# Kernel tuning notes

Measured on AMD Instinct MI355X. Metric: run time of the kernel, lower is better.

## Reference

```python
import jax, jax.numpy as jnp
import numpy as np

CODEBOOK_SIZE = 8192
D_LATENT = 512
COMMITMENT_COST = 0.25


def setup_inputs() -> dict:
    key = jax.random.key(0)
    k1, k2 = jax.random.split(key)
    z = jax.random.normal(k1, (4, 2048, D_LATENT), dtype=jnp.float32)
    # embedding initialized uniform(-1/K, 1/K) in the original; scale a normal draw similarly
    W = jax.random.uniform(k2, (CODEBOOK_SIZE, D_LATENT), dtype=jnp.float32,
                           minval=-1.0 / CODEBOOK_SIZE, maxval=1.0 / CODEBOOK_SIZE)
    return {"z": z, "W": W}


def reference(z, W):
    # Eval-mode forward (no EMA buffer mutation): quantize, straight-through, losses.
    B, S, D = z.shape
    K = W.shape[0]
    z_flat = z.reshape(-1, D)  # [N, D]

    # squared-euclidean distances: ||z||^2 - 2 z W^T + ||w||^2  -> [N, K]
    distances = (jnp.sum(z_flat * z_flat, axis=-1, keepdims=True)
                 - 2.0 * (z_flat @ W.T)
                 + jnp.sum(W * W, axis=-1))
    indices = jnp.argmin(distances, axis=-1)  # [N] int
    z_q = W[indices]  # [N, D] gather

    commitment_loss = jnp.mean((z_flat - jax.lax.stop_gradient(z_q)) ** 2)

    # straight-through estimator
    quantized = z_flat + jax.lax.stop_gradient(z_q - z_flat)

    # perplexity over codebook usage
    counts = jnp.zeros((K,), dtype=jnp.float32).at[indices].add(1.0)
    avg_probs = counts / z_flat.shape[0]
    perplexity = jnp.exp(-jnp.sum(avg_probs * jnp.log(avg_probs + 1e-10)))

    quantized = quantized.reshape(B, S, D)
    indices = indices.reshape(B, S)
    return (quantized, indices, COMMITMENT_COST * commitment_loss, perplexity)
```

## Files before the change

### kernel.cpp

```cpp
#include <hip/hip_runtime.h>
#include <math.h>


typedef __attribute__((ext_vector_type(8))) _Float16 f16x8;
typedef __attribute__((ext_vector_type(16))) float f32x16;

constexpr int N_ROWS = 8192;
constexpr int K_CODES = 8192;
constexpr int D_DIM = 512;
constexpr float COMMIT = 0.25f;
constexpr float EPS = 3.0e-4f;

constexpr size_t OFF_LOSS    = 0;
constexpr size_t OFF_COUNTS  = 64;
constexpr size_t OFF_PARTIAL = 8256;
constexpr size_t OFF_ZZ      = 16384;
constexpr size_t OFF_WW      = 24576;
constexpr size_t OFF_BESTD   = 32768;
constexpr size_t OFF_BESTI   = 2129920;
constexpr size_t F16_BASE_BYTES = 16908288;
constexpr size_t SPLIT_ELEMS = (size_t)8192 * 512;
constexpr size_t SPLIT_BYTES = SPLIT_ELEMS * 2;
constexpr size_t WS_NEED = F16_BASE_BYTES + 2 * SPLIT_BYTES;

constexpr int SPLITK = 8;
constexpr int KSPL = K_CODES / SPLITK;

#define MFMA16(a, b, c) __builtin_amdgcn_mfma_f32_32x32x16_f16((a), (b), (c), 0, 0, 0)

__device__ __forceinline__ bool lexless(float da, int ia, float db, int ib) {
  return da < db || (da == db && ia < ib);
}

__global__ __launch_bounds__(256) void prep_kernel(
    const float* __restrict__ z, const float* __restrict__ W,
    unsigned short* __restrict__ zh, unsigned short* __restrict__ wh,
    float* __restrict__ ws_f) {
  const int src = blockIdx.y;
  const int tid = threadIdx.x;
  if (src == 0 && blockIdx.x < 11) {
#pragma unroll
    for (int k = 0; k < 4; k++) {
      const int idx = blockIdx.x * 1024 + k * 256 + tid;
      if (idx < 10304) ws_f[idx] = 0.0f;
    }
  }
  const float* S = src ? W : z;
  unsigned short* H = src ? wh : zh;
  const float scale = src ? 8192.0f : 1.0f;
  float* norm = ws_f + (src ? OFF_WW : OFF_ZZ);

  const int row = blockIdx.x * 64 + (tid >> 2);
  const int q = tid & 3;
  const float* sp = S + (size_t)row * D_DIM + q * 128;
  const size_t tbase = (size_t)(row >> 7) * 16 * 4096 + (size_t)(row & 127) * 8;

  float4 ssv = {0.f, 0.f, 0.f, 0.f};
#pragma unroll
  for (int c = 0; c < 16; c++) {
    const float4 x = *(const float4*)&sp[c * 8];
    const float4 y = *(const float4*)&sp[c * 8 + 4];
    ssv.x += x.x * x.x; ssv.y += x.y * x.y; ssv.z += x.z * x.z; ssv.w += x.w * x.w;
    ssv.x += y.x * y.x; ssv.y += y.y * y.y; ssv.z += y.z * y.z; ssv.w += y.w * y.w;
    f16x8 hv;
    hv[0] = (_Float16)(x.x * scale); hv[1] = (_Float16)(x.y * scale);
    hv[2] = (_Float16)(x.z * scale); hv[3] = (_Float16)(x.w * scale);
    hv[4] = (_Float16)(y.x * scale); hv[5] = (_Float16)(y.y * scale);
    hv[6] = (_Float16)(y.z * scale); hv[7] = (_Float16)(y.w * scale);
    const int d = q * 128 + c * 8;
    const int dt = d >> 5;
    const int chunk = (d >> 3) & 3;
    *(f16x8*)&H[tbase + (size_t)dt * 4096 + (size_t)chunk * 1024] = hv;
  }
  float s = (ssv.x + ssv.y) + (ssv.z + ssv.w);
  s += __shfl_xor(s, 1, 64);
  s += __shfl_xor(s, 2, 64);
  if (q == 0) norm[row] = s;
}

__global__ __launch_bounds__(256, 2) void vq_screen_kernel(
    const unsigned short* __restrict__ zh_s, const unsigned short* __restrict__ wh_s,
    const float* __restrict__ ww,
    float* __restrict__ bestd2, int* __restrict__ besti2) {
  const int tid = threadIdx.x;
  const int bid = blockIdx.x;
  const int xcd = bid & 7;
  const int j = bid >> 3;
  const int stid = xcd * 8 + (j >> 6);
  const int wi = j & 63;
  const int cb = (stid & 7) * 8 + (wi & 7);
  const int rb = (stid >> 3) * 8 + (wi >> 3);

  const int lane = tid & 63, wv = tid >> 6;
  const int wr = wv >> 1, wc = wv & 1;
  const int lrow = lane & 31, lhi = lane >> 5;

  const f16x8* zh8 = (const f16x8*)zh_s;
  const f16x8* wh8 = (const f16x8*)wh_s;
  const int wbase = wr * 64 + lrow;
  const int zbase = wc * 64 + lrow;

  f32x16 acc[2][2];
#pragma unroll
  for (int i = 0; i < 2; i++)
#pragma unroll
    for (int jj = 0; jj < 2; jj++)
#pragma unroll
      for (int e = 0; e < 16; e++) acc[i][jj][e] = 0.0f;

  f16x8 wA[4], zA[4], wB[4], zB[4];

#define LOADB(WX, ZX, dt) { \
    const int wt_ = (cb * 16 + (dt)) * 512; \
    const int zt_ = (rb * 16 + (dt)) * 512; \
    _Pragma("unroll") \
    for (int ks = 0; ks < 2; ks++) { \
      const int ch_ = ks * 2 + lhi; \
      WX[ks*2+0] = wh8[wt_ + ch_*128 + wbase]; \
      WX[ks*2+1] = wh8[wt_ + ch_*128 + wbase + 32]; \
      ZX[ks*2+0] = zh8[zt_ + ch_*128 + zbase]; \
      ZX[ks*2+1] = zh8[zt_ + ch_*128 + zbase + 32]; \
    } }

#define COMPUTEB(WX, ZX) { \
    __builtin_amdgcn_s_setprio(1); \
    _Pragma("unroll") \
    for (int ks = 0; ks < 2; ks++) { \
      acc[0][0] = MFMA16(WX[ks*2+0], ZX[ks*2+0], acc[0][0]); \
      acc[0][1] = MFMA16(WX[ks*2+0], ZX[ks*2+1], acc[0][1]); \
      acc[1][0] = MFMA16(WX[ks*2+1], ZX[ks*2+0], acc[1][0]); \
      acc[1][1] = MFMA16(WX[ks*2+1], ZX[ks*2+1], acc[1][1]); \
    } \
    __builtin_amdgcn_s_setprio(0); }

  LOADB(wA, zA, 0);
#pragma unroll
  for (int dtp = 0; dtp < 8; dtp++) {
    LOADB(wB, zB, dtp * 2 + 1);
    COMPUTEB(wA, zA);
    if (dtp < 7) LOADB(wA, zA, dtp * 2 + 2);
    COMPUTEB(wB, zB);
  }
#undef LOADB
#undef COMPUTEB

#pragma unroll
  for (int cf = 0; cf < 2; cf++) {
    float p1d = 3.4e38f, p2d = 3.4e38f;
    int   p1i = 0x7fffffff, p2i = 0x7fffffff;
#pragma unroll
    for (int rf = 0; rf < 2; rf++) {
      const int cbase = cb * 128 + wr * 64 + rf * 32 + 4 * lhi;
#pragma unroll
      for (int reg = 0; reg < 16; reg++) {
        const int ci = cbase + (reg & 3) + 8 * (reg >> 2);
        const float d = fmaf(acc[rf][cf][reg], -2.44140625e-4f, ww[ci]);
        const bool b1 = d < p1d;
        const bool b2 = d < p2d;
        p2d = b1 ? p1d : (b2 ? d : p2d);
        p2i = b1 ? p1i : (b2 ? ci : p2i);
        p1d = b1 ? d : p1d;
        p1i = b1 ? ci : p1i;
      }
    }
    const float q1d = __shfl_xor(p1d, 32, 64); const int q1i = __shfl_xor(p1i, 32, 64);
    const float q2d = __shfl_xor(p2d, 32, 64); const int q2i = __shfl_xor(p2i, 32, 64);
    float t1d, t2d; int t1i, t2i;
    if (q1d < p1d) {
      t1d = q1d; t1i = q1i;
      if (p1d < q2d) { t2d = p1d; t2i = p1i; } else { t2d = q2d; t2i = q2i; }
    } else {
      t1d = p1d; t1i = p1i;
      if (q1d < p2d) { t2d = q1d; t2i = q1i; } else { t2d = p2d; t2i = p2i; }
    }
    if (lhi == 0) {
      const int row = rb * 128 + wc * 64 + cf * 32 + lrow;
      const size_t o = (size_t)row * 256 + (size_t)(cb * 2 + wr) * 2;
      float2 dv2; dv2.x = t1d; dv2.y = t2d;
      int2   iv2; iv2.x = t1i; iv2.y = t2i;
      *(float2*)&bestd2[o] = dv2;
      *(int2*)&besti2[o]   = iv2;
    }
  }
}

__global__ __launch_bounds__(256) void vq_rescore_kernel(
    const float* __restrict__ z, const float* __restrict__ W,
    const float* __restrict__ zz, const float* __restrict__ ww,
    const float* __restrict__ bestd2, const int* __restrict__ besti2,
    float* __restrict__ out, float* __restrict__ ws_f) {
  const int row  = (blockIdx.x * 256 + threadIdx.x) >> 6;
  const int lane = threadIdx.x & 63;
  const size_t base = (size_t)row * 256;
  const float4 dv = *(const float4*)&bestd2[base + lane * 4];
  const int4  iv = *(const int4*)&besti2[base + lane * 4];
  float dd[4] = {dv.x, dv.y, dv.z, dv.w};
  int   ii[4] = {iv.x, iv.y, iv.z, iv.w};

  float m = fminf(fminf(dd[0], dd[1]), fminf(dd[2], dd[3]));
#pragma unroll
  for (int mm = 1; mm <= 32; mm <<= 1) m = fminf(m, __shfl_xor(m, mm, 64));
  const float thr = m + EPS;

  const float* zp = z + (size_t)row * D_DIM;
  const float4 za = *(const float4*)&zp[lane * 8];
  const float4 zb = *(const float4*)&zp[lane * 8 + 4];
  const float zzr = zz[row];

  float bd = 3.4e38f; int bi = 0x7fffffff;
#pragma unroll
  for (int s = 0; s < 4; s++) {
    unsigned long long mset = __ballot(dd[s] <= thr);
    while (mset) {
      const int b = __ffsll((long long)mset) - 1;
      mset &= mset - 1;
      const int c = __shfl(ii[s], b, 64);
      const float* wp = W + (size_t)c * D_DIM;
      const float4 wa = *(const float4*)&wp[lane * 8];
      const float4 wb = *(const float4*)&wp[lane * 8 + 4];
      float dot = za.x*wa.x + za.y*wa.y + za.z*wa.z + za.w*wa.w
                + zb.x*wb.x + zb.y*wb.y + zb.z*wb.z + zb.w*wb.w;
#pragma unroll
      for (int mm = 1; mm <= 32; mm <<= 1) dot += __shfl_xor(dot, mm, 64);
      const float dist = (zzr - 2.0f * dot) + ww[c];
      if (dist < bd || (dist == bd && c < bi)) { bd = dist; bi = c; }
    }
  }

  if (lane == 0) {
    out[(size_t)N_ROWS * D_DIM + row] = (float)bi;
    atomicAdd(&ws_f[OFF_COUNTS + bi], 1.0f);
  }
  const float* wp = W + (size_t)bi * D_DIM;
  float* op = out + (size_t)row * D_DIM;
  float lsum = 0.f;
#pragma unroll
  for (int h = 0; h < 2; h++) {
    const int dd2 = h * 256 + lane * 4;
    const float4 zv = *(const float4*)&zp[dd2];
    const float4 wv = *(const float4*)&wp[dd2];
    float4 q;
    q.x = zv.x + (wv.x - zv.x);
    q.y = zv.y + (wv.y - zv.y);
    q.z = zv.z + (wv.z - zv.z);
    q.w = zv.w + (wv.w - zv.w);
    *(float4*)&op[dd2] = q;
    float dx;
    dx = zv.x - wv.x; lsum += dx * dx;
    dx = zv.y - wv.y; lsum += dx * dx;
    dx = zv.z - wv.z; lsum += dx * dx;
    dx = zv.w - wv.w; lsum += dx * dx;
  }
#pragma unroll
  for (int off = 32; off > 0; off >>= 1) lsum += __shfl_down(lsum, off, 64);
  __shared__ float lred[4];
  if (lane == 0) lred[threadIdx.x >> 6] = lsum;
  __syncthreads();
  if (threadIdx.x == 0)
    ws_f[OFF_PARTIAL + blockIdx.x] = lred[0] + lred[1] + lred[2] + lred[3];
}

__global__ __launch_bounds__(256) void rowss_kernel(const float* __restrict__ src,
                                                    float* __restrict__ dst) {
  int row  = (blockIdx.x * 256 + threadIdx.x) >> 6;
  int lane = threadIdx.x & 63;
  const float* p = src + (size_t)row * D_DIM;
  float4 a = *(const float4*)&p[lane * 4];
  float4 b = *(const float4*)&p[256 + lane * 4];
  float s = a.x*a.x + a.y*a.y + a.z*a.z + a.w*a.w
          + b.x*b.x + b.y*b.y + b.z*b.z + b.w*b.w;
#pragma unroll
  for (int off = 32; off > 0; off >>= 1) s += __shfl_down(s, off, 64);
  if (lane == 0) dst[row] = s;
}

constexpr int BN = 64, BK = 64, BD = 32;
__global__ __launch_bounds__(256) void vq_dist_kernel(
    const float* __restrict__ z, const float* __restrict__ W,
    const float* __restrict__ zz, const float* __restrict__ ww,
    float* __restrict__ bestd_out, int* __restrict__ besti_out) {
  __shared__ float zs[BD][68];
  __shared__ float ws_[BD][68];
  __shared__ float rd[BN][16];
  __shared__ int   ri[BN][16];
  const int tid = threadIdx.x;
  const int tx = tid & 15;
  const int ty = tid >> 4;
  const int r0 = blockIdx.x * BN;
  const int kbase0 = blockIdx.y * KSPL;
  const int lr = tid >> 3;
  const int lc = tid & 7;
  float bd[4]; int bi[4];
#pragma unroll
  for (int i = 0; i < 4; i++) { bd[i] = 3.4e38f; bi[i] = 0x7fffffff; }
  float zzr[4];
#pragma unroll
  for (int i = 0; i < 4; i++) zzr[i] = zz[r0 + ty * 4 + i];
  for (int kt = 0; kt < KSPL; kt += BK) {
    const int kb = kbase0 + kt;
    float c[4][4];
#pragma unroll
    for (int i = 0; i < 4; i++)
#pragma unroll
      for (int jj = 0; jj < 4; jj++) c[i][jj] = 0.f;
    for (int dtt = 0; dtt < D_DIM; dtt += BD) {
#pragma unroll
      for (int h = 0; h < 2; h++) {
        const int r = lr + h * 32;
        const float4 v = *(const float4*)&z[(size_t)(r0 + r) * D_DIM + dtt + lc * 4];
        zs[lc*4+0][r] = v.x; zs[lc*4+1][r] = v.y; zs[lc*4+2][r] = v.z; zs[lc*4+3][r] = v.w;
        const float4 u = *(const float4*)&W[(size_t)(kb + r) * D_DIM + dtt + lc * 4];
        ws_[lc*4+0][r] = u.x; ws_[lc*4+1][r] = u.y; ws_[lc*4+2][r] = u.z; ws_[lc*4+3][r] = u.w;
      }
      __syncthreads();
#pragma unroll
      for (int d = 0; d < BD; d++) {
        const float4 a = *(const float4*)&zs[d][ty * 4];
        const float4 b = *(const float4*)&ws_[d][tx * 4];
        c[0][0] += a.x*b.x; c[0][1] += a.x*b.y; c[0][2] += a.x*b.z; c[0][3] += a.x*b.w;
        c[1][0] += a.y*b.x; c[1][1] += a.y*b.y; c[1][2] += a.y*b.z; c[1][3] += a.y*b.w;
        c[2][0] += a.z*b.x; c[2][1] += a.z*b.y; c[2][2] += a.z*b.z; c[2][3] += a.z*b.w;
        c[3][0] += a.w*b.x; c[3][1] += a.w*b.y; c[3][2] += a.w*b.z; c[3][3] += a.w*b.w;
      }
      __syncthreads();
    }
#pragma unroll
    for (int i = 0; i < 4; i++) {
#pragma unroll
      for (int jj = 0; jj < 4; jj++) {
        const int col = kb + tx * 4 + jj;
        const float dist = (zzr[i] - 2.0f * c[i][jj]) + ww[col];
        if (dist < bd[i]) { bd[i] = dist; bi[i] = col; }
      }
    }
  }
#pragma unroll
  for (int i = 0; i < 4; i++) { rd[ty * 4 + i][tx] = bd[i]; ri[ty * 4 + i][tx] = bi[i]; }
  __syncthreads();
  if (tid < BN) {
    float best = rd[tid][0]; int bidx = ri[tid][0];
#pragma unroll
    for (int t = 1; t < 16; t++) {
      const float dv = rd[tid][t]; const int iv = ri[tid][t];
      if (dv < best || (dv == best && iv < bidx)) { best = dv; bidx = iv; }
    }
    bestd_out[(size_t)blockIdx.y * N_ROWS + r0 + tid] = best;
    besti_out[(size_t)blockIdx.y * N_ROWS + r0 + tid] = bidx;
  }
}

__global__ __launch_bounds__(256) void vq_gather8_kernel(
    const float* __restrict__ z, const float* __restrict__ W,
    const float* __restrict__ bestd, const int* __restrict__ besti,
    float* __restrict__ out, float* __restrict__ ws_f) {
  const int row  = (blockIdx.x * 256 + threadIdx.x) >> 6;
  const int lane = threadIdx.x & 63;
  int bidx = 0;
  if (lane == 0) {
    float best = bestd[row];
    bidx = besti[row];
#pragma unroll
    for (int s = 1; s < SPLITK; s++) {
      const float dv = bestd[(size_t)s * N_ROWS + row];
      const int iv = besti[(size_t)s * N_ROWS + row];
      if (dv < best || (dv == best && iv < bidx)) { best = dv; bidx = iv; }
    }
    out[(size_t)N_ROWS * D_DIM + row] = (float)bidx;
    atomicAdd(&ws_f[OFF_COUNTS + bidx], 1.0f);
  }
  bidx = __shfl(bidx, 0, 64);
  const float* zp = z + (size_t)row * D_DIM;
  const float* wp = W + (size_t)bidx * D_DIM;
  float* op = out + (size_t)row * D_DIM;
  float lsum = 0.f;
#pragma unroll
  for (int h = 0; h < 2; h++) {
    const int d = h * 256 + lane * 4;
    const float4 zv = *(const float4*)&zp[d];
    const float4 wv = *(const float4*)&wp[d];
    float4 q;
    q.x = zv.x + (wv.x - zv.x);
    q.y = zv.y + (wv.y - zv.y);
    q.z = zv.z + (wv.z - zv.z);
    q.w = zv.w + (wv.w - zv.w);
    *(float4*)&op[d] = q;
    float dx;
    dx = zv.x - wv.x; lsum += dx * dx;
    dx = zv.y - wv.y; lsum += dx * dx;
    dx = zv.z - wv.z; lsum += dx * dx;
    dx = zv.w - wv.w; lsum += dx * dx;
  }
#pragma unroll
  for (int off = 32; off > 0; off >>= 1) lsum += __shfl_down(lsum, off, 64);
  if (lane == 0) atomicAdd(&ws_f[OFF_LOSS], lsum);
}

__global__ __launch_bounds__(256) void vq_finalize_kernel(const float* __restrict__ ws_f,
                                                          float* __restrict__ out,
                                                          int use_partial) {
  const int tid = threadIdx.x;
  float ls = 0.f;
  if (use_partial) {
    for (int i = tid; i < 2048; i += 256) ls += ws_f[OFF_PARTIAL + i];
  }
  float s = 0.f;
  for (int k = tid; k < K_CODES; k += 256) {
    const float p = ws_f[OFF_COUNTS + k] * (1.0f / 8192.0f);
    s += p * logf(p + 1e-10f);
  }
#pragma unroll
  for (int off = 32; off > 0; off >>= 1) {
    s  += __shfl_down(s, off, 64);
    ls += __shfl_down(ls, off, 64);
  }
  __shared__ float red[4], redl[4];
  if ((tid & 63) == 0) { red[tid >> 6] = s; redl[tid >> 6] = ls; }
  __syncthreads();
  if (tid == 0) {
    const float tot = red[0] + red[1] + red[2] + red[3];
    const float L = use_partial ? (redl[0] + redl[1] + redl[2] + redl[3])
                                : ws_f[OFF_LOSS];
    out[(size_t)N_ROWS * D_DIM + N_ROWS]     = COMMIT * (L / 4194304.0f);
    out[(size_t)N_ROWS * D_DIM + N_ROWS + 1] = expf(-tot);
  }
}

extern "C" void kernel_launch(void* const* d_in, const int* in_sizes, int n_in,
                              void* d_out, int out_size, void* d_ws, size_t ws_size,
                              hipStream_t stream) {
  const float* z = (const float*)d_in[0];
  const float* W = (const float*)d_in[1];
  float* out = (float*)d_out;
  float* ws_f = (float*)d_ws;
  int* ws_i = (int*)d_ws;

  if (ws_size >= WS_NEED) {
    unsigned short* zh = (unsigned short*)((char*)d_ws + F16_BASE_BYTES);
    unsigned short* wh = zh + SPLIT_ELEMS;
    prep_kernel<<<dim3(128, 2), 256, 0, stream>>>(z, W, zh, wh, ws_f);
    vq_screen_kernel<<<4096, 256, 0, stream>>>(
        zh, wh, ws_f + OFF_WW, ws_f + OFF_BESTD, ws_i + OFF_BESTI);
    vq_rescore_kernel<<<N_ROWS / 4, 256, 0, stream>>>(
        z, W, ws_f + OFF_ZZ, ws_f + OFF_WW,
        ws_f + OFF_BESTD, ws_i + OFF_BESTI, out, ws_f);
    vq_finalize_kernel<<<1, 256, 0, stream>>>(ws_f, out, 1);
  } else {
    hipMemsetAsync(d_ws, 0, (OFF_COUNTS + K_CODES) * sizeof(float), stream);
    rowss_kernel<<<N_ROWS / 4, 256, 0, stream>>>(z, ws_f + OFF_ZZ);
    rowss_kernel<<<K_CODES / 4, 256, 0, stream>>>(W, ws_f + OFF_WW);
    dim3 grid(N_ROWS / BN, SPLITK);
    vq_dist_kernel<<<grid, 256, 0, stream>>>(z, W, ws_f + OFF_ZZ, ws_f + OFF_WW,
                                             ws_f + OFF_BESTD, ws_i + OFF_BESTI);
    vq_gather8_kernel<<<N_ROWS / 4, 256, 0, stream>>>(z, W, ws_f + OFF_BESTD,
                                                      ws_i + OFF_BESTI, out, ws_f);
    vq_finalize_kernel<<<1, 256, 0, stream>>>(ws_f, out, 0);
  }
}
```

Measured before the change: 216.7 us.

## Enlarge screen tile to 128x256, drop XCD swizzle and manual double-buffering

The fp16 screening GEMM now gives each block 128 codes by 256 rows: each wave holds a 2x4 grid of MFMA accumulators instead of 2x2, and the grid is halved to 2048 blocks. This reuses each loaded W fragment across more z fragments, cutting global load traffic per FLOP. The XCD-aware block-to-tile remapping is replaced by a plain linear mapping, and the explicit A/B register double-buffering is replaced by a simple loop unrolled by 2 that leaves scheduling to the compiler. In exchange, accumulator register pressure doubles, which may lower occupancy against the launch bound of 2, and L2 locality across XCDs may get worse.

```diff
diff --git a/kernel.cpp b/kernel.cpp
--- a/kernel.cpp
+++ b/kernel.cpp
@@ -27,10 +27,6 @@
 constexpr int KSPL = K_CODES / SPLITK;
 
 #define MFMA16(a, b, c) __builtin_amdgcn_mfma_f32_32x32x16_f16((a), (b), (c), 0, 0, 0)
-
-__device__ __forceinline__ bool lexless(float da, int ia, float db, int ib) {
-  return da < db || (da == db && ia < ib);
-}
 
 __global__ __launch_bounds__(256) void prep_kernel(
     const float* __restrict__ z, const float* __restrict__ W,
@@ -84,12 +80,8 @@
     float* __restrict__ bestd2, int* __restrict__ besti2) {
   const int tid = threadIdx.x;
   const int bid = blockIdx.x;
-  const int xcd = bid & 7;
-  const int j = bid >> 3;
-  const int stid = xcd * 8 + (j >> 6);
-  const int wi = j & 63;
-  const int cb = (stid & 7) * 8 + (wi & 7);
-  const int rb = (stid >> 3) * 8 + (wi >> 3);
+  const int cb = bid & 63;
+  const int rb = bid >> 6;
 
   const int lane = tid & 63, wv = tid >> 6;
   const int wr = wv >> 1, wc = wv & 1;
@@ -98,54 +90,43 @@
   const f16x8* zh8 = (const f16x8*)zh_s;
   const f16x8* wh8 = (const f16x8*)wh_s;
   const int wbase = wr * 64 + lrow;
-  const int zbase = wc * 64 + lrow;
-
-  f32x16 acc[2][2];
+  const int ztile = rb * 2 + wc;
+
+  f32x16 acc[2][4];
 #pragma unroll
   for (int i = 0; i < 2; i++)
 #pragma unroll
-    for (int jj = 0; jj < 2; jj++)
+    for (int jj = 0; jj < 4; jj++)
 #pragma unroll
       for (int e = 0; e < 16; e++) acc[i][jj][e] = 0.0f;
 
-  f16x8 wA[4], zA[4], wB[4], zB[4];
-
-#define LOADB(WX, ZX, dt) { \
-    const int wt_ = (cb * 16 + (dt)) * 512; \
-    const int zt_ = (rb * 16 + (dt)) * 512; \
-    _Pragma("unroll") \
-    for (int ks = 0; ks < 2; ks++) { \
-      const int ch_ = ks * 2 + lhi; \
-      WX[ks*2+0] = wh8[wt_ + ch_*128 + wbase]; \
-      WX[ks*2+1] = wh8[wt_ + ch_*128 + wbase + 32]; \
-      ZX[ks*2+0] = zh8[zt_ + ch_*128 + zbase]; \
-      ZX[ks*2+1] = zh8[zt_ + ch_*128 + zbase + 32]; \
-    } }
-
-#define COMPUTEB(WX, ZX) { \
-    __builtin_amdgcn_s_setprio(1); \
-    _Pragma("unroll") \
-    for (int ks = 0; ks < 2; ks++) { \
-      acc[0][0] = MFMA16(WX[ks*2+0], ZX[ks*2+0], acc[0][0]); \
-      acc[0][1] = MFMA16(WX[ks*2+0], ZX[ks*2+1], acc[0][1]); \
-      acc[1][0] = MFMA16(WX[ks*2+1], ZX[ks*2+0], acc[1][0]); \
-      acc[1][1] = MFMA16(WX[ks*2+1], ZX[ks*2+1], acc[1][1]); \
-    } \
-    __builtin_amdgcn_s_setprio(0); }
-
-  LOADB(wA, zA, 0);
-#pragma unroll
-  for (int dtp = 0; dtp < 8; dtp++) {
-    LOADB(wB, zB, dtp * 2 + 1);
-    COMPUTEB(wA, zA);
-    if (dtp < 7) LOADB(wA, zA, dtp * 2 + 2);
-    COMPUTEB(wB, zB);
-  }
-#undef LOADB
-#undef COMPUTEB
-
-#pragma unroll
-  for (int cf = 0; cf < 2; cf++) {
+#pragma unroll 2
+  for (int dt = 0; dt < 16; dt++) {
+    const int wt_ = (cb * 16 + dt) * 512;
+    const int zt_ = (ztile * 16 + dt) * 512;
+    f16x8 wf[2][2], zf[2][4];
+#pragma unroll
+    for (int ks = 0; ks < 2; ks++) {
+      const int ch = ks * 2 + lhi;
+      wf[ks][0] = wh8[wt_ + ch * 128 + wbase];
+      wf[ks][1] = wh8[wt_ + ch * 128 + wbase + 32];
+#pragma unroll
+      for (int cf = 0; cf < 4; cf++)
+        zf[ks][cf] = zh8[zt_ + ch * 128 + cf * 32 + lrow];
+    }
+    __builtin_amdgcn_s_setprio(1);
+#pragma unroll
+    for (int ks = 0; ks < 2; ks++)
+#pragma unroll
+      for (int cf = 0; cf < 4; cf++) {
+        acc[0][cf] = MFMA16(wf[ks][0], zf[ks][cf], acc[0][cf]);
+        acc[1][cf] = MFMA16(wf[ks][1], zf[ks][cf], acc[1][cf]);
+      }
+    __builtin_amdgcn_s_setprio(0);
+  }
+
+#pragma unroll
+  for (int cf = 0; cf < 4; cf++) {
     float p1d = 3.4e38f, p2d = 3.4e38f;
     int   p1i = 0x7fffffff, p2i = 0x7fffffff;
 #pragma unroll
@@ -174,7 +155,7 @@
       if (q1d < p2d) { t2d = q1d; t2i = q1i; } else { t2d = p2d; t2i = p2i; }
     }
     if (lhi == 0) {
-      const int row = rb * 128 + wc * 64 + cf * 32 + lrow;
+      const int row = rb * 256 + wc * 128 + cf * 32 + lrow;
       const size_t o = (size_t)row * 256 + (size_t)(cb * 2 + wr) * 2;
       float2 dv2; dv2.x = t1d; dv2.y = t2d;
       int2   iv2; iv2.x = t1i; iv2.y = t2i;
@@ -438,7 +419,7 @@
     unsigned short* zh = (unsigned short*)((char*)d_ws + F16_BASE_BYTES);
     unsigned short* wh = zh + SPLIT_ELEMS;
     prep_kernel<<<dim3(128, 2), 256, 0, stream>>>(z, W, zh, wh, ws_f);
-    vq_screen_kernel<<<4096, 256, 0, stream>>>(
+    vq_screen_kernel<<<2048, 256, 0, stream>>>(
         zh, wh, ws_f + OFF_WW, ws_f + OFF_BESTD, ws_i + OFF_BESTI);
     vq_rescore_kernel<<<N_ROWS / 4, 256, 0, stream>>>(
         z, W, ws_f + OFF_ZZ, ws_f + OFF_WW,
```

New measurement: 199.5 us. 7.9% less time.
